# Kernel tuning notes

Measured on AMD Instinct MI355X. Metric: run time of the kernel, lower is better.

## Reference

```python
import jax, jax.numpy as jnp
import numpy as np

B, S, D, H, DFF, G = 2, 2048, 1024, 16, 4096, 64
HD = D // H  # seq_dimensions = d_model // num_heads
SCALE = 1.0 / np.sqrt(HD).astype(np.float32)


def _ln(x, g, b):
    m = x.mean(-1, keepdims=True)
    v = x.var(-1, keepdims=True)
    return (x - m) / jnp.sqrt(v + 1e-5) * g + b


def _mha(q_in, k_in, v_in, wq, bq, wk, bk, wv, bv, wo, bo, mask):
    Bq, Sq, _ = q_in.shape
    Sk = k_in.shape[1]
    def proj(t, w, b):
        return (t @ w + b).reshape(t.shape[0], t.shape[1], H, HD).transpose(0, 2, 1, 3)
    q = proj(q_in, wq, bq)  # [B,H,Sq,HD]
    k = proj(k_in, wk, bk)
    v = proj(v_in, wv, bv)
    scores = jnp.einsum('bhqd,bhkd->bhqk', q, k) * SCALE
    if mask is not None:
        scores = jnp.where(mask, scores, jnp.float32(-1e9))
    a = jax.nn.softmax(scores, axis=-1)
    o = jnp.einsum('bhqk,bhkd->bhqd', a, v).transpose(0, 2, 1, 3).reshape(Bq, Sq, D)
    return o @ wo + bo


def setup_inputs() -> dict:
    key = jax.random.key(0)
    ks = jax.random.split(key, 32)
    w = lambda i, shape: jax.random.normal(ks[i], shape, jnp.float32) * 0.02
    z = lambda shape: jnp.zeros(shape, jnp.float32)
    # BigBird-style mask: causal + global (first G tokens) + G random cols per row
    rng = np.random.default_rng(0)
    mask = np.tril(np.ones((S, S), dtype=bool))
    mask[:, :G] = True
    mask[:G, :] = True
    rand_cols = rng.integers(0, S, size=(S, G))
    mask[np.arange(S)[:, None], rand_cols] = True
    return dict(
        cur_input=jax.random.normal(ks[0], (B, S, D), jnp.float32),
        classVector=jax.random.normal(ks[1], (B, 1, 10), jnp.float32),
        attn_mask=jnp.asarray(mask),
        sa_wq=w(2, (D, D)), sa_bq=z(D), sa_wk=w(3, (D, D)), sa_bk=z(D),
        sa_wv=w(4, (D, D)), sa_bv=z(D), sa_wo=w(5, (D, D)), sa_bo=z(D),
        ln1_g=jnp.ones(D, jnp.float32), ln1_b=z(D),
        ce_w=w(6, (10, D)), ce_b=z(D),
        ca_wq=w(7, (D, D)), ca_bq=z(D), ca_wk=w(8, (D, D)), ca_bk=z(D),
        ca_wv=w(9, (D, D)), ca_bv=z(D), ca_wo=w(10, (D, D)), ca_bo=z(D),
        ln2_g=jnp.ones(D, jnp.float32), ln2_b=z(D),
        ff_w1=w(11, (D, DFF)), ff_b1=z(DFF), ff_w2=w(12, (DFF, D)), ff_b2=z(D),
        ln3_g=jnp.ones(D, jnp.float32), ln3_b=z(D),
    )


def reference(cur_input, classVector, attn_mask,
              sa_wq, sa_bq, sa_wk, sa_bk, sa_wv, sa_bv, sa_wo, sa_bo, ln1_g, ln1_b,
              ce_w, ce_b,
              ca_wq, ca_bq, ca_wk, ca_bk, ca_wv, ca_bv, ca_wo, ca_bo, ln2_g, ln2_b,
              ff_w1, ff_b1, ff_w2, ff_b2, ln3_g, ln3_b):
    # AddNorm(masked rand+global self-attn)
    sa = _mha(cur_input, cur_input, cur_input,
              sa_wq, sa_bq, sa_wk, sa_bk, sa_wv, sa_bv, sa_wo, sa_bo, attn_mask)
    h = _ln(cur_input + sa, ln1_g, ln1_b)
    # class vector embedding -> cross-attn K/V
    cv = classVector @ ce_w + ce_b  # [B,1,D]
    ca = _mha(h, cv, cv, ca_wq, ca_bq, ca_wk, ca_bk, ca_wv, ca_bv, ca_wo, ca_bo, None)
    h2 = _ln(h + ca, ln2_g, ln2_b)
    # AddNorm(FFN)
    ff = jax.nn.relu(h2 @ ff_w1 + ff_b1) @ ff_w2 + ff_b2
    return _ln(h2 + ff, ln3_g, ln3_b)
```

## Files before the change

kernel.cpp:

```cpp
#include <hip/hip_runtime.h>
#include <hip/hip_bf16.h>
#include <stdint.h>

#define S_LEN 2048
#define DMODEL 1024
#define NHEAD 16
#define BATCH 2

typedef __bf16 bf16x8 __attribute__((ext_vector_type(8)));
typedef __bf16 bf16x4 __attribute__((ext_vector_type(4)));
typedef float f32x4 __attribute__((ext_vector_type(4)));

__device__ __forceinline__ void gll16(const void* gsrc, void* ldst) {
  auto g = (const __attribute__((address_space(1))) unsigned int*)(uintptr_t)gsrc;
  auto l = (__attribute__((address_space(3))) unsigned int*)(uint32_t)(uintptr_t)ldst;
  __builtin_amdgcn_global_load_lds(g, l, 16, 0, 0);
}

__device__ __forceinline__ void wt_core(const float* __restrict__ W, __bf16* __restrict__ Wt,
                                        int Kd, int Nd, int bx, int by) {
  __shared__ __bf16 tile[64 * 72];
  const int n0 = bx * 64, k0 = by * 64;
  const int t = threadIdx.x;
#pragma unroll
  for (int i = 0; i < 16; ++i) {
    int idx = t + 256 * i;
    int r = idx >> 6, c = idx & 63;
    tile[r * 72 + c] = (__bf16)W[(size_t)(k0 + r) * Nd + n0 + c];
  }
  __syncthreads();
#pragma unroll
  for (int i = 0; i < 2; ++i) {
    int ch = t + 256 * i;
    int r = ch >> 3, c0 = (ch & 7) * 8;
    bf16x8 v;
#pragma unroll
    for (int j = 0; j < 8; ++j) v[j] = tile[(c0 + j) * 72 + r];
    *(bf16x8*)&Wt[(size_t)(n0 + r) * Kd + k0 + c0] = v;
  }
}

__global__ __launch_bounds__(256) void wt4_kernel(const float* w0, const float* w1,
                                                  const float* w2, const float* w3, __bf16* o0,
                                                  __bf16* o1, __bf16* o2, __bf16* o3) {
  const int z = blockIdx.z;
  const float* W = (z == 0) ? w0 : (z == 1) ? w1 : (z == 2) ? w2 : w3;
  __bf16* Wt = (z == 0) ? o0 : (z == 1) ? o1 : (z == 2) ? o2 : o3;
  wt_core(W, Wt, 1024, 1024, blockIdx.x, blockIdx.y);
}

__global__ __launch_bounds__(256) void wt2_kernel(const float* w1, const float* w2, __bf16* o1,
                                                  __bf16* o2) {
  if (blockIdx.z == 0)
    wt_core(w1, o1, 1024, 4096, blockIdx.x, blockIdx.y);
  else
    wt_core(w2, o2, 4096, 1024, blockIdx.y, blockIdx.x);
}

__global__ __launch_bounds__(256) void tobf_kernel(const float* __restrict__ x,
                                                   __bf16* __restrict__ y, int n4) {
  const int stride = gridDim.x * 256;
  for (int i = blockIdx.x * 256 + threadIdx.x; i < n4; i += stride) {
    float4 v = ((const float4*)x)[i];
    bf16x4 o = {(__bf16)v.x, (__bf16)v.y, (__bf16)v.z, (__bf16)v.w};
    *(bf16x4*)(y + (size_t)i * 4) = o;
  }
}

__global__ __launch_bounds__(256) void maskbits_kernel(const uint8_t* __restrict__ m8,
                                                       unsigned long long* __restrict__ mb) {
  const int idx = blockIdx.x * 256 + threadIdx.x;
  const int r = idx >> 5, c = idx & 31;
  const bool u8 = (m8[1] != 0);
  unsigned long long bits = 0;
  if (u8) {
    const unsigned long long* p = (const unsigned long long*)(m8 + (size_t)r * 2048 + c * 64);
#pragma unroll
    for (int i = 0; i < 8; ++i) {
      unsigned long long wq = p[i];
#pragma unroll
      for (int j = 0; j < 8; ++j)
        if ((wq >> (8 * j)) & 0xFFull) bits |= 1ull << (i * 8 + j);
    }
  } else {
    const int* p = (const int*)m8 + (size_t)r * 2048 + (size_t)c * 64;
#pragma unroll
    for (int i = 0; i < 64; ++i)
      if (p[i] != 0) bits |= 1ull << i;
  }
  mb[(size_t)r * 32 + c] = bits;
}

__device__ __forceinline__ void gemm_core(const __bf16* __restrict__ A,
                                          const __bf16* __restrict__ Bt,
                                          const float* __restrict__ bias,
                                          float* __restrict__ outF, __bf16* __restrict__ outB,
                                          bool relu, float scale, int N, int K) {
  __shared__ __bf16 As[2][128 * 64];
  __shared__ __bf16 Bs[2][128 * 64];
  const int t = threadIdx.x;
  const int l = t & 63, w = t >> 6;
  const int wr = w >> 1, wc = w & 1;
  const int gx = gridDim.x;
  const int lin = blockIdx.x + gx * blockIdx.y;
  const int cpx = (gx * gridDim.y) >> 3;
  const int s = (lin & 7) * cpx + (lin >> 3);
  const int bx = s % gx, by = s / gx;
  const int l15 = l & 15, l4 = l >> 4;
  f32x4 acc[4][4] = {};
  const size_t arow = (size_t)by * 128;
  const size_t brow = (size_t)bx * 128;

  auto stage = [&](int d, int k0) {
#pragma unroll
    for (int i = 0; i < 4; ++i) {
      int c = t + 256 * i;
      int r = c >> 3, sl = c & 7;
      int kk = (sl ^ (r & 7)) << 3;
      gll16(A + (arow + r) * K + k0 + kk, (char*)As[d] + (size_t)c * 16);
      gll16(Bt + (brow + r) * K + k0 + kk, (char*)Bs[d] + (size_t)c * 16);
    }
  };

  stage(0, 0);
  asm volatile("s_waitcnt vmcnt(0)" ::: "memory");
  __builtin_amdgcn_s_barrier();
  int cur = 0;
  for (int k0 = 0; k0 < K; k0 += 64) {
    if (k0 + 64 < K) stage(cur ^ 1, k0 + 64);
#pragma unroll
    for (int kk = 0; kk < 2; ++kk) {
      bf16x8 af[4], bfr[4];
#pragma unroll
      for (int m = 0; m < 4; ++m) {
        int row = wr * 64 + m * 16 + l15, vs = kk * 4 + l4;
        af[m] = *(const bf16x8*)((char*)As[cur] + row * 128 + ((vs ^ (row & 7)) << 4));
      }
#pragma unroll
      for (int n = 0; n < 4; ++n) {
        int row = wc * 64 + n * 16 + l15, vs = kk * 4 + l4;
        bfr[n] = *(const bf16x8*)((char*)Bs[cur] + row * 128 + ((vs ^ (row & 7)) << 4));
      }
#pragma unroll
      for (int m = 0; m < 4; ++m)
#pragma unroll
        for (int n = 0; n < 4; ++n)
          acc[m][n] = __builtin_amdgcn_mfma_f32_16x16x32_bf16(af[m], bfr[n], acc[m][n], 0, 0, 0);
    }
    asm volatile("s_waitcnt vmcnt(0)" ::: "memory");
    __builtin_amdgcn_s_barrier();
    cur ^= 1;
  }
  const int r0 = by * 128 + wr * 64, c0 = bx * 128 + wc * 64;
#pragma unroll
  for (int m = 0; m < 4; ++m) {
#pragma unroll
    for (int n = 0; n < 4; ++n) {
      int col = c0 + n * 16 + l15;
      float bv = bias ? bias[col] : 0.0f;
#pragma unroll
      for (int i = 0; i < 4; ++i) {
        int row = r0 + m * 16 + l4 * 4 + i;
        float v = (acc[m][n][i] + bv) * scale;
        if (relu) v = fmaxf(v, 0.0f);
        if (outF) outF[(size_t)row * N + col] = v;
        if (outB) outB[(size_t)row * N + col] = (__bf16)v;
      }
    }
  }
}

__global__ __launch_bounds__(256) void gemm_kernel(const __bf16* A, const __bf16* Bt,
                                                   const float* bias, float* outF, __bf16* outB,
                                                   int relu, float scale, int N, int K) {
  gemm_core(A, Bt, bias, outF, outB, relu != 0, scale, N, K);
}

__global__ __launch_bounds__(256) void gemm_qkv_kernel(const __bf16* __restrict__ A,
                                                       const __bf16* __restrict__ WT3,
                                                       const float* bq, const float* bk,
                                                       const float* bv, __bf16* Qo, __bf16* Ko,
                                                       __bf16* Vo) {
  __shared__ __bf16 As[2][128 * 64];
  __shared__ __bf16 Bs[2][128 * 64];
  const int t = threadIdx.x;
  const int l = t & 63, w = t >> 6;
  const int wr = w >> 1, wc = w & 1;
  const int gx = gridDim.x;
  const int lin = blockIdx.x + gx * blockIdx.y;
  const int cpx = (gx * gridDim.y) >> 3;
  const int s = (lin & 7) * cpx + (lin >> 3);
  const int bx = s % gx, by = s / gx;
  const int l15 = l & 15, l4 = l >> 4;
  const int K = 1024;
  f32x4 acc[4][4] = {};
  const size_t arow = (size_t)by * 128;
  const size_t brow = (size_t)bx * 128;

  auto stage = [&](int d, int k0) {
#pragma unroll
    for (int i = 0; i < 4; ++i) {
      int c = t + 256 * i;
      int r = c >> 3, sl = c & 7;
      int kk = (sl ^ (r & 7)) << 3;
      gll16(A + (arow + r) * K + k0 + kk, (char*)As[d] + (size_t)c * 16);
      gll16(WT3 + (brow + r) * K + k0 + kk, (char*)Bs[d] + (size_t)c * 16);
    }
  };

  stage(0, 0);
  asm volatile("s_waitcnt vmcnt(0)" ::: "memory");
  __builtin_amdgcn_s_barrier();
  int cur = 0;
  for (int k0 = 0; k0 < K; k0 += 64) {
    if (k0 + 64 < K) stage(cur ^ 1, k0 + 64);
#pragma unroll
    for (int kk = 0; kk < 2; ++kk) {
      bf16x8 af[4], bfr[4];
#pragma unroll
      for (int m = 0; m < 4; ++m) {
        int row = wr * 64 + m * 16 + l15, vs = kk * 4 + l4;
        af[m] = *(const bf16x8*)((char*)As[cur] + row * 128 + ((vs ^ (row & 7)) << 4));
      }
#pragma unroll
      for (int n = 0; n < 4; ++n) {
        int row = wc * 64 + n * 16 + l15, vs = kk * 4 + l4;
        bfr[n] = *(const bf16x8*)((char*)Bs[cur] + row * 128 + ((vs ^ (row & 7)) << 4));
      }
#pragma unroll
      for (int m = 0; m < 4; ++m)
#pragma unroll
        for (int n = 0; n < 4; ++n)
          acc[m][n] = __builtin_amdgcn_mfma_f32_16x16x32_bf16(af[m], bfr[n], acc[m][n], 0, 0, 0);
    }
    asm volatile("s_waitcnt vmcnt(0)" ::: "memory");
    __builtin_amdgcn_s_barrier();
    cur ^= 1;
  }
  const int z = bx >> 3;
  __bf16* out = (z == 0) ? Qo : (z == 1) ? Ko : Vo;
  const float* bias = (z == 0) ? bq : (z == 1) ? bk : bv;
  const float scale = (z == 0) ? 0.125f : 1.0f;
  const int r0 = by * 128 + wr * 64, c0 = (bx & 7) * 128 + wc * 64;
#pragma unroll
  for (int m = 0; m < 4; ++m) {
#pragma unroll
    for (int n = 0; n < 4; ++n) {
      int col = c0 + n * 16 + l15;
      float bvv = bias[col];
#pragma unroll
      for (int i = 0; i < 4; ++i) {
        int row = r0 + m * 16 + l4 * 4 + i;
        out[(size_t)row * DMODEL + col] = (__bf16)((acc[m][n][i] + bvv) * scale);
      }
    }
  }
}

__global__ __launch_bounds__(256) void vt_kernel(const __bf16* __restrict__ V,
                                                 __bf16* __restrict__ Vt) {
  __shared__ __bf16 tile[64 * 72];
  const int sb = blockIdx.x, h = blockIdx.y, b = blockIdx.z;
  const int t = threadIdx.x;
#pragma unroll
  for (int i = 0; i < 2; ++i) {
    int ch = t + 256 * i;
    int r = ch >> 3, c0 = (ch & 7) * 8;
    *(bf16x8*)&tile[r * 72 + c0] =
        *(const bf16x8*)&V[(size_t)(b * S_LEN + sb * 64 + r) * DMODEL + h * 64 + c0];
  }
  __syncthreads();
#pragma unroll
  for (int i = 0; i < 2; ++i) {
    int ch = t + 256 * i;
    int r = ch >> 3, c0 = (ch & 7) * 8;
    bf16x8 v;
#pragma unroll
    for (int j = 0; j < 8; ++j) v[j] = tile[(c0 + j) * 72 + r];
    *(bf16x8*)&Vt[((size_t)((b * NHEAD + h) * 64) + r) * S_LEN + sb * 64 + c0] = v;
  }
}

__global__ __launch_bounds__(256, 4) void flash_kernel(const __bf16* __restrict__ Q,
                                                       const __bf16* __restrict__ K,
                                                       const __bf16* __restrict__ Vt,
                                                       const unsigned long long* __restrict__ mbits,
                                                       __bf16* __restrict__ O) {
  __shared__ char smem[40 * 1024];
  const int lin = blockIdx.x + 32 * (blockIdx.y + 16 * blockIdx.z);
  const int xr = lin & 7, xm = lin >> 3;
  const int g = xr + 8 * (xm & 3);
  const int qb = xm >> 2;
  const int h = g & 15, b = g >> 4;
  const int t = threadIdx.x, w = t >> 6, l = t & 63;
  const int l15 = l & 15, l4 = l >> 4;
  const int q_glob = qb * 64 + w * 16 + l15;

#pragma unroll
  for (int i = 0; i < 2; ++i) {
    int c = t + 256 * i;
    int r = c >> 3, p = c & 7;
    int vsl = p ^ (r & 7);
    gll16(Q + (size_t)(b * S_LEN + qb * 64 + r) * DMODEL + h * 64 + vsl * 8,
          smem + (size_t)c * 16);
    gll16(K + (size_t)(b * S_LEN + r) * DMODEL + h * 64 + vsl * 8, smem + 8192 + (size_t)c * 16);
    gll16(Vt + (size_t)((b * NHEAD + h) * 64 + r) * S_LEN + vsl * 8, smem + 24576 + (size_t)c * 16);
  }
  __syncthreads();

  bf16x8 aq[2];
#pragma unroll
  for (int ks = 0; ks < 2; ++ks) {
    int row = w * 16 + l15, vs = ks * 4 + l4;
    aq[ks] = *(const bf16x8*)(smem + row * 128 + ((vs ^ (row & 7)) << 4));
  }
  char* PsW = smem + w * 2048;

  f32x4 o[4] = {};
  float mrow = -INFINITY, lrow = 0.f;
  unsigned long long mb_cur = 0, mb_next = 0;
  int cur = 0;
  for (int kt = 0; kt < 32; ++kt) {
    char* Kc = smem + 8192 + cur * 8192;
    char* Vc = smem + 24576 + cur * 8192;
    if (kt < 31) {
      char* Kn = smem + 8192 + (cur ^ 1) * 8192;
      char* Vn = smem + 24576 + (cur ^ 1) * 8192;
#pragma unroll
      for (int i = 0; i < 2; ++i) {
        int c = t + 256 * i;
        int r = c >> 3, p = c & 7;
        int vsl = p ^ (r & 7);
        gll16(K + (size_t)(b * S_LEN + (kt + 1) * 64 + r) * DMODEL + h * 64 + vsl * 8,
              Kn + (size_t)c * 16);
        gll16(Vt + (size_t)((b * NHEAD + h) * 64 + r) * S_LEN + (kt + 1) * 64 + vsl * 8,
              Vn + (size_t)c * 16);
      }
      mb_next = mbits[(size_t)q_glob * 32 + kt + 1];
    }
    f32x4 s[4] = {};
#pragma unroll
    for (int ks = 0; ks < 2; ++ks)
#pragma unroll
      for (int n = 0; n < 4; ++n) {
        int row = n * 16 + l15, vs = ks * 4 + l4;
        bf16x8 kf = *(const bf16x8*)(Kc + row * 128 + ((vs ^ (row & 7)) << 4));
        s[n] = __builtin_amdgcn_mfma_f32_16x16x32_bf16(kf, aq[ks], s[n], 0, 0, 0);
      }
    const bool skip = (kt < qb) || (kt == 0) || (qb == 0);
    float tmax = s[0][0];
#pragma unroll
    for (int n = 0; n < 4; ++n)
#pragma unroll
      for (int i = 0; i < 4; ++i) tmax = fmaxf(tmax, s[n][i]);
    tmax = fmaxf(tmax, __shfl_xor(tmax, 16));
    tmax = fmaxf(tmax, __shfl_xor(tmax, 32));
    if (__ballot(tmax > mrow)) {
      const float nm = fmaxf(mrow, tmax);
      const float alpha = __expf(mrow - nm);
      mrow = nm;
      lrow *= alpha;
#pragma unroll
      for (int i = 0; i < 4; ++i) {
        float ai = __shfl(alpha, (l & 48) | (l4 * 4 + i));
#pragma unroll
        for (int n = 0; n < 4; ++n) o[n][i] *= ai;
      }
    }
    float pv[4][4];
#pragma unroll
    for (int n = 0; n < 4; ++n)
#pragma unroll
      for (int i = 0; i < 4; ++i) pv[n][i] = __expf(s[n][i] - mrow);
    if (!skip) {
#pragma unroll
      for (int n = 0; n < 4; ++n) {
        unsigned int mB = (unsigned int)(mb_cur >> (n * 16 + l4 * 4));
#pragma unroll
        for (int i = 0; i < 4; ++i)
          if (!((mB >> i) & 1)) pv[n][i] = 0.f;
      }
    }
    float tsum = 0.f;
#pragma unroll
    for (int n = 0; n < 4; ++n)
#pragma unroll
      for (int i = 0; i < 4; ++i) tsum += pv[n][i];
    tsum += __shfl_xor(tsum, 16);
    tsum += __shfl_xor(tsum, 32);
    lrow += tsum;
#pragma unroll
    for (int n = 0; n < 4; ++n) {
      bf16x4 pk = {(__bf16)pv[n][0], (__bf16)pv[n][1], (__bf16)pv[n][2], (__bf16)pv[n][3]};
      int slot = n * 4 + l4;
      *(bf16x4*)(PsW + l15 * 128 + ((slot ^ l15) & 15) * 8) = pk;
    }
#pragma unroll
    for (int ks = 0; ks < 2; ++ks) {
      int s0 = (ks * 8 + l4 * 2) ^ l15;
      int s1 = (ks * 8 + l4 * 2 + 1) ^ l15;
      bf16x4 pa0 = *(const bf16x4*)(PsW + l15 * 128 + (s0 & 15) * 8);
      bf16x4 pa1 = *(const bf16x4*)(PsW + l15 * 128 + (s1 & 15) * 8);
      bf16x8 ap = {pa0[0], pa0[1], pa0[2], pa0[3], pa1[0], pa1[1], pa1[2], pa1[3]};
#pragma unroll
      for (int n = 0; n < 4; ++n) {
        int vrow = n * 16 + l15, vvs = ks * 4 + l4;
        bf16x8 bv = *(const bf16x8*)(Vc + vrow * 128 + ((vvs ^ (vrow & 7)) << 4));
        o[n] = __builtin_amdgcn_mfma_f32_16x16x32_bf16(ap, bv, o[n], 0, 0, 0);
      }
    }
    asm volatile("s_waitcnt vmcnt(0)" ::: "memory");
    __builtin_amdgcn_s_barrier();
    mb_cur = mb_next;
    cur ^= 1;
  }
#pragma unroll
  for (int i = 0; i < 4; ++i) {
    float li = __shfl(lrow, (l & 48) | (l4 * 4 + i));
    float rli = 1.0f / li;
#pragma unroll
    for (int n = 0; n < 4; ++n)
      O[(size_t)(b * S_LEN + qb * 64 + w * 16 + l4 * 4 + i) * DMODEL + h * 64 + n * 16 + l15] =
          (__bf16)(o[n][i] * rli);
  }
}

__global__ __launch_bounds__(256) void ln_kernel(const float* __restrict__ x,
                                                 const float* __restrict__ res,
                                                 const float* __restrict__ resvec,
                                                 const float* __restrict__ g,
                                                 const float* __restrict__ beta,
                                                 float* __restrict__ outF,
                                                 __bf16* __restrict__ outB) {
  const int row = blockIdx.x;
  const int b = row >> 11;
  const int t = threadIdx.x;
  float4 v = ((const float4*)(x + (size_t)row * DMODEL))[t];
  if (res) {
    float4 r = ((const float4*)(res + (size_t)row * DMODEL))[t];
    v.x += r.x; v.y += r.y; v.z += r.z; v.w += r.w;
  }
  if (resvec) {
    float4 r = ((const float4*)(resvec + (size_t)b * DMODEL))[t];
    v.x += r.x; v.y += r.y; v.z += r.z; v.w += r.w;
  }
  float s1 = v.x + v.y + v.z + v.w;
  float s2 = v.x * v.x + v.y * v.y + v.z * v.z + v.w * v.w;
#pragma unroll
  for (int off = 32; off; off >>= 1) {
    s1 += __shfl_xor(s1, off);
    s2 += __shfl_xor(s2, off);
  }
  __shared__ float red[8];
  const int w = t >> 6, l = t & 63;
  if (l == 0) { red[w] = s1; red[4 + w] = s2; }
  __syncthreads();
  s1 = red[0] + red[1] + red[2] + red[3];
  s2 = red[4] + red[5] + red[6] + red[7];
  const float mean = s1 * (1.0f / DMODEL);
  const float var = s2 * (1.0f / DMODEL) - mean * mean;
  const float rstd = rsqrtf(var + 1e-5f);
  float4 gg = ((const float4*)g)[t];
  float4 bb = ((const float4*)beta)[t];
  float4 o;
  o.x = (v.x - mean) * rstd * gg.x + bb.x;
  o.y = (v.y - mean) * rstd * gg.y + bb.y;
  o.z = (v.z - mean) * rstd * gg.z + bb.z;
  o.w = (v.w - mean) * rstd * gg.w + bb.w;
  if (outF) ((float4*)(outF + (size_t)row * DMODEL))[t] = o;
  if (outB) {
    bf16x4 p = {(__bf16)o.x, (__bf16)o.y, (__bf16)o.z, (__bf16)o.w};
    *(bf16x4*)(outB + (size_t)row * DMODEL + t * 4) = p;
  }
}

__global__ __launch_bounds__(256) void cv_kernel(const float* __restrict__ cls,
                                                 const float* __restrict__ cw,
                                                 const float* __restrict__ cb,
                                                 float* __restrict__ cv) {
  const int i = blockIdx.x * 256 + threadIdx.x;
  const int b = i >> 10, d = i & 1023;
  float s = cb[d];
#pragma unroll
  for (int j = 0; j < 10; ++j) s += cls[b * 10 + j] * cw[j * DMODEL + d];
  cv[i] = s;
}

__global__ __launch_bounds__(256) void matvec_part_kernel(const float* __restrict__ x,
                                                          const float* __restrict__ W,
                                                          float* __restrict__ part) {
  const int c = blockIdx.x, b = blockIdx.y;
  const int t = threadIdx.x;
  float4 acc = {0.f, 0.f, 0.f, 0.f};
  const int k0 = c * 16;
#pragma unroll
  for (int k = 0; k < 16; ++k) {
    float xv = x[b * DMODEL + k0 + k];
    float4 wv = ((const float4*)(W + (size_t)(k0 + k) * DMODEL))[t];
    acc.x += xv * wv.x; acc.y += xv * wv.y; acc.z += xv * wv.z; acc.w += xv * wv.w;
  }
  ((float4*)(part + ((size_t)(b * 64 + c)) * DMODEL))[t] = acc;
}

__global__ __launch_bounds__(256) void matvec_red_kernel(const float* __restrict__ part,
                                                         const float* __restrict__ bias,
                                                         float* __restrict__ out) {
  const int b = blockIdx.y;
  const int t = threadIdx.x;
  float4 acc = ((const float4*)bias)[t];
#pragma unroll 8
  for (int c = 0; c < 64; ++c) {
    float4 p = ((const float4*)(part + ((size_t)(b * 64 + c)) * DMODEL))[t];
    acc.x += p.x; acc.y += p.y; acc.z += p.z; acc.w += p.w;
  }
  ((float4*)(out + (size_t)b * DMODEL))[t] = acc;
}

extern "C" void kernel_launch(void* const* d_in, const int* in_sizes, int n_in, void* d_out,
                              int out_size, void* d_ws, size_t ws_size, hipStream_t stream) {
  (void)in_sizes; (void)n_in; (void)out_size; (void)ws_size;
  const float* cur = (const float*)d_in[0];
  const float* cls = (const float*)d_in[1];
  const uint8_t* msk = (const uint8_t*)d_in[2];
  const float* sa_wq = (const float*)d_in[3];
  const float* sa_bq = (const float*)d_in[4];
  const float* sa_wk = (const float*)d_in[5];
  const float* sa_bk = (const float*)d_in[6];
  const float* sa_wv = (const float*)d_in[7];
  const float* sa_bv = (const float*)d_in[8];
  const float* sa_wo = (const float*)d_in[9];
  const float* sa_bo = (const float*)d_in[10];
  const float* ln1_g = (const float*)d_in[11];
  const float* ln1_b = (const float*)d_in[12];
  const float* ce_w = (const float*)d_in[13];
  const float* ce_b = (const float*)d_in[14];
  const float* ca_wv = (const float*)d_in[19];
  const float* ca_bv = (const float*)d_in[20];
  const float* ca_wo = (const float*)d_in[21];
  const float* ca_bo = (const float*)d_in[22];
  const float* ln2_g = (const float*)d_in[23];
  const float* ln2_b = (const float*)d_in[24];
  const float* ff_w1 = (const float*)d_in[25];
  const float* ff_b1 = (const float*)d_in[26];
  const float* ff_w2 = (const float*)d_in[27];
  const float* ff_b2 = (const float*)d_in[28];
  const float* ln3_g = (const float*)d_in[29];
  const float* ln3_b = (const float*)d_in[30];

  char* ws = (char*)d_ws;
  const size_t MB = 1ull << 20;
  __bf16* WQT = (__bf16*)(ws + 0 * MB);
  __bf16* WKT = (__bf16*)(ws + 2 * MB);
  __bf16* WVT = (__bf16*)(ws + 4 * MB);
  __bf16* WOT = (__bf16*)(ws + 6 * MB);
  __bf16* W1T = (__bf16*)(ws + 8 * MB);
  __bf16* W2T = (__bf16*)(ws + 16 * MB);
  __bf16* XBF = (__bf16*)(ws + 24 * MB);
  __bf16* QBF = (__bf16*)(ws + 32 * MB);
  __bf16* KBF = (__bf16*)(ws + 40 * MB);
  __bf16* VBF = (__bf16*)(ws + 48 * MB);
  __bf16* VTT = (__bf16*)(ws + 56 * MB);
  __bf16* F1 = (__bf16*)(ws + 32 * MB);
  float* ATT = (float*)(ws + 64 * MB);
  float* HF = (float*)(ws + 80 * MB);
  float* H2F = (float*)(ws + 96 * MB);
  __bf16* H2B = (__bf16*)(ws + 112 * MB);
  float* CVV = (float*)(ws + 120 * MB);
  float* VV = (float*)(ws + 120 * MB + 65536);
  float* CAV = (float*)(ws + 120 * MB + 131072);
  unsigned long long* MBITS = (unsigned long long*)(ws + 121 * MB);
  float* MVP = (float*)(ws + 122 * MB);

  dim3 blk(256);
  maskbits_kernel<<<dim3(256), blk, 0, stream>>>(msk, MBITS);
  wt4_kernel<<<dim3(16, 16, 4), blk, 0, stream>>>(sa_wq, sa_wk, sa_wv, sa_wo, WQT, WKT, WVT, WOT);
  wt2_kernel<<<dim3(64, 16, 2), blk, 0, stream>>>(ff_w1, ff_w2, W1T, W2T);
  tobf_kernel<<<dim3(2048), blk, 0, stream>>>(cur, XBF, 1048576);
  gemm_qkv_kernel<<<dim3(24, 32), blk, 0, stream>>>(XBF, WQT, sa_bq, sa_bk, sa_bv, QBF, KBF, VBF);
  vt_kernel<<<dim3(32, 16, 2), blk, 0, stream>>>(VBF, VTT);
  flash_kernel<<<dim3(32, 16, 2), blk, 0, stream>>>(QBF, KBF, VTT, MBITS, XBF);
  gemm_kernel<<<dim3(8, 32), blk, 0, stream>>>(XBF, WOT, sa_bo, ATT, nullptr, 0, 1.0f, 1024, 1024);
  ln_kernel<<<dim3(4096), blk, 0, stream>>>(cur, ATT, nullptr, ln1_g, ln1_b, HF, nullptr);
  cv_kernel<<<dim3(8), blk, 0, stream>>>(cls, ce_w, ce_b, CVV);
  matvec_part_kernel<<<dim3(64, 2), blk, 0, stream>>>(CVV, ca_wv, MVP);
  matvec_red_kernel<<<dim3(1, 2), blk, 0, stream>>>(MVP, ca_bv, VV);
  matvec_part_kernel<<<dim3(64, 2), blk, 0, stream>>>(VV, ca_wo, MVP);
  matvec_red_kernel<<<dim3(1, 2), blk, 0, stream>>>(MVP, ca_bo, CAV);
  ln_kernel<<<dim3(4096), blk, 0, stream>>>(HF, nullptr, CAV, ln2_g, ln2_b, H2F, H2B);
  gemm_kernel<<<dim3(32, 32), blk, 0, stream>>>(H2B, W1T, ff_b1, nullptr, F1, 1, 1.0f, 4096, 1024);
  gemm_kernel<<<dim3(8, 32), blk, 0, stream>>>(F1, W2T, ff_b2, ATT, nullptr, 0, 1.0f, 1024, 4096);
  ln_kernel<<<dim3(4096), blk, 0, stream>>>(H2F, ATT, nullptr, ln3_g, ln3_b, (float*)d_out,
                                            nullptr);
}
```

Measured before the change: 314.3 us.

## Merge prep kernels, add 128x64 GEMM for N=1024, setprio around MFMAs

Folds the mask-bit packing, the weight transposes and the input bf16 conversion into one prep kernel launch. Adds a 128x64-tile GEMM for the two N=1024 projections so they launch 512 blocks instead of 256 and fill more of the CUs. Raises wave priority around the MFMA blocks in the flash kernel, and fuses the class-vector embedding into the first matvec_part kernel. Together these cut launch count and improve occupancy, at the cost of less data reuse per tile in the smaller GEMM.

```diff
diff --git a/kernel.cpp b/kernel.cpp
--- a/kernel.cpp
+++ b/kernel.cpp
@@ -40,55 +40,56 @@
   }
 }
 
-__global__ __launch_bounds__(256) void wt4_kernel(const float* w0, const float* w1,
-                                                  const float* w2, const float* w3, __bf16* o0,
-                                                  __bf16* o1, __bf16* o2, __bf16* o3) {
-  const int z = blockIdx.z;
-  const float* W = (z == 0) ? w0 : (z == 1) ? w1 : (z == 2) ? w2 : w3;
-  __bf16* Wt = (z == 0) ? o0 : (z == 1) ? o1 : (z == 2) ? o2 : o3;
-  wt_core(W, Wt, 1024, 1024, blockIdx.x, blockIdx.y);
-}
-
-__global__ __launch_bounds__(256) void wt2_kernel(const float* w1, const float* w2, __bf16* o1,
-                                                  __bf16* o2) {
-  if (blockIdx.z == 0)
-    wt_core(w1, o1, 1024, 4096, blockIdx.x, blockIdx.y);
-  else
-    wt_core(w2, o2, 4096, 1024, blockIdx.y, blockIdx.x);
-}
-
-__global__ __launch_bounds__(256) void tobf_kernel(const float* __restrict__ x,
-                                                   __bf16* __restrict__ y, int n4) {
-  const int stride = gridDim.x * 256;
-  for (int i = blockIdx.x * 256 + threadIdx.x; i < n4; i += stride) {
-    float4 v = ((const float4*)x)[i];
-    bf16x4 o = {(__bf16)v.x, (__bf16)v.y, (__bf16)v.z, (__bf16)v.w};
-    *(bf16x4*)(y + (size_t)i * 4) = o;
-  }
-}
-
-__global__ __launch_bounds__(256) void maskbits_kernel(const uint8_t* __restrict__ m8,
-                                                       unsigned long long* __restrict__ mb) {
-  const int idx = blockIdx.x * 256 + threadIdx.x;
-  const int r = idx >> 5, c = idx & 31;
-  const bool u8 = (m8[1] != 0);
-  unsigned long long bits = 0;
-  if (u8) {
-    const unsigned long long* p = (const unsigned long long*)(m8 + (size_t)r * 2048 + c * 64);
-#pragma unroll
-    for (int i = 0; i < 8; ++i) {
-      unsigned long long wq = p[i];
-#pragma unroll
-      for (int j = 0; j < 8; ++j)
-        if ((wq >> (8 * j)) & 0xFFull) bits |= 1ull << (i * 8 + j);
-    }
+__global__ __launch_bounds__(256) void prep_kernel(
+    const uint8_t* __restrict__ m8, unsigned long long* __restrict__ mb, const float* w0,
+    const float* w1, const float* w2, const float* w3, __bf16* o0, __bf16* o1, __bf16* o2,
+    __bf16* o3, const float* fw1, const float* fw2, __bf16* fo1, __bf16* fo2,
+    const float* __restrict__ x, __bf16* __restrict__ y) {
+  const int bid = blockIdx.x;
+  const int t = threadIdx.x;
+  if (bid < 256) {
+    const int idx = bid * 256 + t;
+    const int r = idx >> 5, c = idx & 31;
+    const bool u8 = (m8[1] != 0);
+    unsigned long long bits = 0;
+    if (u8) {
+      const unsigned long long* p = (const unsigned long long*)(m8 + (size_t)r * 2048 + c * 64);
+#pragma unroll
+      for (int i = 0; i < 8; ++i) {
+        unsigned long long wq = p[i];
+#pragma unroll
+        for (int j = 0; j < 8; ++j)
+          if ((wq >> (8 * j)) & 0xFFull) bits |= 1ull << (i * 8 + j);
+      }
+    } else {
+      const int* p = (const int*)m8 + (size_t)r * 2048 + (size_t)c * 64;
+#pragma unroll
+      for (int i = 0; i < 64; ++i)
+        if (p[i] != 0) bits |= 1ull << i;
+    }
+    mb[(size_t)r * 32 + c] = bits;
+  } else if (bid < 1280) {
+    const int local = bid - 256;
+    const int z = local >> 8, lb = local & 255;
+    const float* W = (z == 0) ? w0 : (z == 1) ? w1 : (z == 2) ? w2 : w3;
+    __bf16* Wt = (z == 0) ? o0 : (z == 1) ? o1 : (z == 2) ? o2 : o3;
+    wt_core(W, Wt, 1024, 1024, lb & 15, lb >> 4);
+  } else if (bid < 2304) {
+    const int lb = bid - 1280;
+    wt_core(fw1, fo1, 1024, 4096, lb & 63, lb >> 6);
+  } else if (bid < 3328) {
+    const int lb = bid - 2304;
+    wt_core(fw2, fo2, 4096, 1024, lb >> 6, lb & 63);
   } else {
-    const int* p = (const int*)m8 + (size_t)r * 2048 + (size_t)c * 64;
-#pragma unroll
-    for (int i = 0; i < 64; ++i)
-      if (p[i] != 0) bits |= 1ull << i;
-  }
-  mb[(size_t)r * 32 + c] = bits;
+    const int lb = bid - 3328;
+#pragma unroll
+    for (int j = 0; j < 4; ++j) {
+      int i = lb * 1024 + j * 256 + t;
+      float4 v = ((const float4*)x)[i];
+      bf16x4 o = {(__bf16)v.x, (__bf16)v.y, (__bf16)v.z, (__bf16)v.w};
+      *(bf16x4*)(y + (size_t)i * 4) = o;
+    }
+  }
 }
 
 __device__ __forceinline__ void gemm_core(const __bf16* __restrict__ A,
@@ -174,6 +175,91 @@
                                                    const float* bias, float* outF, __bf16* outB,
                                                    int relu, float scale, int N, int K) {
   gemm_core(A, Bt, bias, outF, outB, relu != 0, scale, N, K);
+}
+
+__global__ __launch_bounds__(256) void gemm64_kernel(const __bf16* __restrict__ A,
+                                                     const __bf16* __restrict__ Bt,
+                                                     const float* __restrict__ bias,
+                                                     float* __restrict__ outF,
+                                                     __bf16* __restrict__ outB, int relu,
+                                                     int N, int K) {
+  __shared__ __bf16 As[2][128 * 64];
+  __shared__ __bf16 Bs[2][64 * 64];
+  const int t = threadIdx.x;
+  const int l = t & 63, w = t >> 6;
+  const int gx = gridDim.x;
+  const int lin = blockIdx.x + gx * blockIdx.y;
+  const int cpx = (gx * gridDim.y) >> 3;
+  const int s = (lin & 7) * cpx + (lin >> 3);
+  const int bx = s % gx, by = s / gx;
+  const int l15 = l & 15, l4 = l >> 4;
+  f32x4 acc[2][4] = {};
+  const size_t arow = (size_t)by * 128;
+  const size_t brow = (size_t)bx * 64;
+
+  auto stage = [&](int d, int k0) {
+#pragma unroll
+    for (int i = 0; i < 4; ++i) {
+      int c = t + 256 * i;
+      int r = c >> 3, sl = c & 7;
+      int kk = (sl ^ (r & 7)) << 3;
+      gll16(A + (arow + r) * K + k0 + kk, (char*)As[d] + (size_t)c * 16);
+    }
+#pragma unroll
+    for (int i = 0; i < 2; ++i) {
+      int c = t + 256 * i;
+      int r = c >> 3, sl = c & 7;
+      int kk = (sl ^ (r & 7)) << 3;
+      gll16(Bt + (brow + r) * K + k0 + kk, (char*)Bs[d] + (size_t)c * 16);
+    }
+  };
+
+  stage(0, 0);
+  asm volatile("s_waitcnt vmcnt(0)" ::: "memory");
+  __builtin_amdgcn_s_barrier();
+  int cur = 0;
+  for (int k0 = 0; k0 < K; k0 += 64) {
+    if (k0 + 64 < K) stage(cur ^ 1, k0 + 64);
+#pragma unroll
+    for (int kk = 0; kk < 2; ++kk) {
+      bf16x8 af[2], bfr[4];
+#pragma unroll
+      for (int m = 0; m < 2; ++m) {
+        int row = w * 32 + m * 16 + l15, vs = kk * 4 + l4;
+        af[m] = *(const bf16x8*)((char*)As[cur] + row * 128 + ((vs ^ (row & 7)) << 4));
+      }
+#pragma unroll
+      for (int n = 0; n < 4; ++n) {
+        int row = n * 16 + l15, vs = kk * 4 + l4;
+        bfr[n] = *(const bf16x8*)((char*)Bs[cur] + row * 128 + ((vs ^ (row & 7)) << 4));
+      }
+#pragma unroll
+      for (int m = 0; m < 2; ++m)
+#pragma unroll
+        for (int n = 0; n < 4; ++n)
+          acc[m][n] = __builtin_amdgcn_mfma_f32_16x16x32_bf16(af[m], bfr[n], acc[m][n], 0, 0, 0);
+    }
+    asm volatile("s_waitcnt vmcnt(0)" ::: "memory");
+    __builtin_amdgcn_s_barrier();
+    cur ^= 1;
+  }
+  const int r0 = by * 128 + w * 32, c0 = bx * 64;
+#pragma unroll
+  for (int m = 0; m < 2; ++m) {
+#pragma unroll
+    for (int n = 0; n < 4; ++n) {
+      int col = c0 + n * 16 + l15;
+      float bv = bias ? bias[col] : 0.0f;
+#pragma unroll
+      for (int i = 0; i < 4; ++i) {
+        int row = r0 + m * 16 + l4 * 4 + i;
+        float v = acc[m][n][i] + bv;
+        if (relu) v = fmaxf(v, 0.0f);
+        if (outF) outF[(size_t)row * N + col] = v;
+        if (outB) outB[(size_t)row * N + col] = (__bf16)v;
+      }
+    }
+  }
 }
 
 __global__ __launch_bounds__(256) void gemm_qkv_kernel(const __bf16* __restrict__ A,
@@ -339,6 +425,7 @@
       mb_next = mbits[(size_t)q_glob * 32 + kt + 1];
     }
     f32x4 s[4] = {};
+    __builtin_amdgcn_s_setprio(1);
 #pragma unroll
     for (int ks = 0; ks < 2; ++ks)
 #pragma unroll
@@ -347,6 +434,7 @@
         bf16x8 kf = *(const bf16x8*)(Kc + row * 128 + ((vs ^ (row & 7)) << 4));
         s[n] = __builtin_amdgcn_mfma_f32_16x16x32_bf16(kf, aq[ks], s[n], 0, 0, 0);
       }
+    __builtin_amdgcn_s_setprio(0);
     const bool skip = (kt < qb) || (kt == 0) || (qb == 0);
     float tmax = s[0][0];
 #pragma unroll
@@ -402,12 +490,14 @@
       bf16x4 pa0 = *(const bf16x4*)(PsW + l15 * 128 + (s0 & 15) * 8);
       bf16x4 pa1 = *(const bf16x4*)(PsW + l15 * 128 + (s1 & 15) * 8);
       bf16x8 ap = {pa0[0], pa0[1], pa0[2], pa0[3], pa1[0], pa1[1], pa1[2], pa1[3]};
+      __builtin_amdgcn_s_setprio(1);
 #pragma unroll
       for (int n = 0; n < 4; ++n) {
         int vrow = n * 16 + l15, vvs = ks * 4 + l4;
         bf16x8 bv = *(const bf16x8*)(Vc + vrow * 128 + ((vvs ^ (vrow & 7)) << 4));
         o[n] = __builtin_amdgcn_mfma_f32_16x16x32_bf16(ap, bv, o[n], 0, 0, 0);
       }
+      __builtin_amdgcn_s_setprio(0);
     }
     asm volatile("s_waitcnt vmcnt(0)" ::: "memory");
     __builtin_amdgcn_s_barrier();
@@ -474,28 +564,31 @@
   }
 }
 
-__global__ __launch_bounds__(256) void cv_kernel(const float* __restrict__ cls,
-                                                 const float* __restrict__ cw,
-                                                 const float* __restrict__ cb,
-                                                 float* __restrict__ cv) {
-  const int i = blockIdx.x * 256 + threadIdx.x;
-  const int b = i >> 10, d = i & 1023;
-  float s = cb[d];
-#pragma unroll
-  for (int j = 0; j < 10; ++j) s += cls[b * 10 + j] * cw[j * DMODEL + d];
-  cv[i] = s;
-}
-
 __global__ __launch_bounds__(256) void matvec_part_kernel(const float* __restrict__ x,
                                                           const float* __restrict__ W,
-                                                          float* __restrict__ part) {
+                                                          float* __restrict__ part,
+                                                          const float* __restrict__ cls,
+                                                          const float* __restrict__ cw,
+                                                          const float* __restrict__ cb) {
   const int c = blockIdx.x, b = blockIdx.y;
   const int t = threadIdx.x;
+  const int k0 = c * 16;
+  __shared__ float xs[16];
+  if (cls) {
+    if (t < 16) {
+      float s = cb[k0 + t];
+#pragma unroll
+      for (int j = 0; j < 10; ++j) s += cls[b * 10 + j] * cw[j * DMODEL + k0 + t];
+      xs[t] = s;
+    }
+  } else {
+    if (t < 16) xs[t] = x[b * DMODEL + k0 + t];
+  }
+  __syncthreads();
   float4 acc = {0.f, 0.f, 0.f, 0.f};
-  const int k0 = c * 16;
 #pragma unroll
   for (int k = 0; k < 16; ++k) {
-    float xv = x[b * DMODEL + k0 + k];
+    float xv = xs[k];
     float4 wv = ((const float4*)(W + (size_t)(k0 + k) * DMODEL))[t];
     acc.x += xv * wv.x; acc.y += xv * wv.y; acc.z += xv * wv.z; acc.w += xv * wv.w;
   }
@@ -565,30 +658,26 @@
   float* HF = (float*)(ws + 80 * MB);
   float* H2F = (float*)(ws + 96 * MB);
   __bf16* H2B = (__bf16*)(ws + 112 * MB);
-  float* CVV = (float*)(ws + 120 * MB);
-  float* VV = (float*)(ws + 120 * MB + 65536);
-  float* CAV = (float*)(ws + 120 * MB + 131072);
+  float* VV = (float*)(ws + 120 * MB);
+  float* CAV = (float*)(ws + 120 * MB + 65536);
   unsigned long long* MBITS = (unsigned long long*)(ws + 121 * MB);
   float* MVP = (float*)(ws + 122 * MB);
 
   dim3 blk(256);
-  maskbits_kernel<<<dim3(256), blk, 0, stream>>>(msk, MBITS);
-  wt4_kernel<<<dim3(16, 16, 4), blk, 0, stream>>>(sa_wq, sa_wk, sa_wv, sa_wo, WQT, WKT, WVT, WOT);
-  wt2_kernel<<<dim3(64, 16, 2), blk, 0, stream>>>(ff_w1, ff_w2, W1T, W2T);
-  tobf_kernel<<<dim3(2048), blk, 0, stream>>>(cur, XBF, 1048576);
+  prep_kernel<<<dim3(4352), blk, 0, stream>>>(msk, MBITS, sa_wq, sa_wk, sa_wv, sa_wo, WQT, WKT,
+                                              WVT, WOT, ff_w1, ff_w2, W1T, W2T, cur, XBF);
   gemm_qkv_kernel<<<dim3(24, 32), blk, 0, stream>>>(XBF, WQT, sa_bq, sa_bk, sa_bv, QBF, KBF, VBF);
   vt_kernel<<<dim3(32, 16, 2), blk, 0, stream>>>(VBF, VTT);
   flash_kernel<<<dim3(32, 16, 2), blk, 0, stream>>>(QBF, KBF, VTT, MBITS, XBF);
-  gemm_kernel<<<dim3(8, 32), blk, 0, stream>>>(XBF, WOT, sa_bo, ATT, nullptr, 0, 1.0f, 1024, 1024);
+  gemm64_kernel<<<dim3(16, 32), blk, 0, stream>>>(XBF, WOT, sa_bo, ATT, nullptr, 0, 1024, 1024);
   ln_kernel<<<dim3(4096), blk, 0, stream>>>(cur, ATT, nullptr, ln1_g, ln1_b, HF, nullptr);
-  cv_kernel<<<dim3(8), blk, 0, stream>>>(cls, ce_w, ce_b, CVV);
-  matvec_part_kernel<<<dim3(64, 2), blk, 0, stream>>>(CVV, ca_wv, MVP);
+  matvec_part_kernel<<<dim3(64, 2), blk, 0, stream>>>(nullptr, ca_wv, MVP, cls, ce_w, ce_b);
   matvec_red_kernel<<<dim3(1, 2), blk, 0, stream>>>(MVP, ca_bv, VV);
-  matvec_part_kernel<<<dim3(64, 2), blk, 0, stream>>>(VV, ca_wo, MVP);
+  matvec_part_kernel<<<dim3(64, 2), blk, 0, stream>>>(VV, ca_wo, MVP, nullptr, nullptr, nullptr);
   matvec_red_kernel<<<dim3(1, 2), blk, 0, stream>>>(MVP, ca_bo, CAV);
   ln_kernel<<<dim3(4096), blk, 0, stream>>>(HF, nullptr, CAV, ln2_g, ln2_b, H2F, H2B);
   gemm_kernel<<<dim3(32, 32), blk, 0, stream>>>(H2B, W1T, ff_b1, nullptr, F1, 1, 1.0f, 4096, 1024);
-  gemm_kernel<<<dim3(8, 32), blk, 0, stream>>>(F1, W2T, ff_b2, ATT, nullptr, 0, 1.0f, 1024, 4096);
+  gemm64_kernel<<<dim3(16, 32), blk, 0, stream>>>(F1, W2T, ff_b2, ATT, nullptr, 0, 1024, 4096);
   ln_kernel<<<dim3(4096), blk, 0, stream>>>(H2F, ATT, nullptr, ln3_g, ln3_b, (float*)d_out,
                                             nullptr);
 }
```

Result: faster. 296.2 us (-5.7%).
